# Optimization experiments

Measured on AMD Instinct MI355X. Metric: run time of the kernel, lower is better.

The kernel has to match this reference:

```python
import jax, jax.numpy as jnp
import numpy as np

EMBED = 1024
HEADS = 16
HEAD_DIM = EMBED // HEADS


def setup_inputs() -> dict:
    key = jax.random.key(0)
    ks = jax.random.split(key, 9)
    B, S, E = 4, 2048, EMBED
    std = 1.0 / np.sqrt(E)  # kaiming_normal fan_in, linear
    xav = np.sqrt(6.0 / (E + E))
    return {
        "x": jax.random.normal(ks[0], (B, S, E), dtype=jnp.float32),
        "Wq": jax.random.normal(ks[1], (E, E), dtype=jnp.float32) * std,
        "bq": jnp.zeros((E,), dtype=jnp.float32),
        "Wk": jax.random.normal(ks[2], (E, E), dtype=jnp.float32) * std,
        "bk": jnp.zeros((E,), dtype=jnp.float32),
        "Wv": jax.random.normal(ks[3], (E, E), dtype=jnp.float32) * std,
        "bv": jnp.zeros((E,), dtype=jnp.float32),
        "Wo": jax.random.uniform(ks[4], (E, E), dtype=jnp.float32, minval=-xav, maxval=xav),
        "bo": jnp.zeros((E,), dtype=jnp.float32),
        "ln_gamma": jnp.ones((E,), dtype=jnp.float32),
        "ln_beta": jnp.zeros((E,), dtype=jnp.float32),
    }


def _layer_norm(x, gamma, beta, eps=1e-5):
    mu = jnp.mean(x, axis=-1, keepdims=True)
    var = jnp.var(x, axis=-1, keepdims=True)
    return (x - mu) * jax.lax.rsqrt(var + eps) * gamma + beta


def reference(x, Wq, bq, Wk, bk, Wv, bv, Wo, bo, ln_gamma, ln_beta):
    B, S, E = x.shape
    residual = x
    h = _layer_norm(x, ln_gamma, ln_beta)
    # torch Linear: y = h @ W.T + b; here W stored as (out, in)
    Q = h @ Wq.T + bq
    K = h @ Wk.T + bk
    V = h @ Wv.T + bv
    # (B, H, S, D)
    def split(t):
        return t.reshape(B, S, HEADS, HEAD_DIM).transpose(0, 2, 1, 3)
    Q, K, V = split(Q), split(K), split(V)
    scale = HEAD_DIM ** -0.5
    scores = jnp.einsum("bhqd,bhkd->bhqk", Q, K) * scale  # (B,H,S,S)
    attn = jax.nn.softmax(scores.astype(jnp.float32), axis=-1).astype(scores.dtype)
    out = jnp.einsum("bhqk,bhkd->bhqd", attn, V)
    out = out.transpose(0, 2, 1, 3).reshape(B, S, E)
    out = out @ Wo.T + bo
    return out + residual
```

## Files before the change

kernel.cpp:

```cpp
#include <hip/hip_runtime.h>
#include <hip/hip_bf16.h>
#include <stdint.h>

#define EMB 1024
#define NH 16
#define HD 64
#define SEQ 2048
#define NB 4

typedef __attribute__((ext_vector_type(8))) short bh8;
typedef __attribute__((ext_vector_type(4))) float f32x4;

#define QSCALE 0.1803368801111f
#define SMAX_NEG -48.0f

__device__ __forceinline__ unsigned short f2bf(float x) {
  union { float f; uint32_t u; } v; v.f = x;
  uint32_t r = v.u + 0x7FFFu + ((v.u >> 16) & 1u);
  return (unsigned short)(r >> 16);
}

__device__ __forceinline__ void async16(void* lds, const void* g) {
  __builtin_amdgcn_global_load_lds(
      (const __attribute__((address_space(1))) uint32_t*)g,
      (__attribute__((address_space(3))) uint32_t*)lds,
      16, 0, 0);
}

#define MFMA_BF16(a, b, c) __builtin_amdgcn_mfma_f32_16x16x32_bf16((a), (b), (c), 0, 0, 0)

__global__ __launch_bounds__(256) void ln_kernel(const float* __restrict__ x,
                                                 const float* __restrict__ gamma,
                                                 const float* __restrict__ beta,
                                                 unsigned short* __restrict__ hout) {
  const int row = blockIdx.x;
  const int t = threadIdx.x;
  const float4 xv = ((const float4*)(x + (size_t)row * EMB))[t];
  float s = xv.x + xv.y + xv.z + xv.w;
  float ss = xv.x * xv.x + xv.y * xv.y + xv.z * xv.z + xv.w * xv.w;
#pragma unroll
  for (int off = 32; off; off >>= 1) {
    s += __shfl_down(s, off);
    ss += __shfl_down(ss, off);
  }
  __shared__ float red[8];
  const int wid = t >> 6, lane = t & 63;
  if (lane == 0) { red[wid] = s; red[4 + wid] = ss; }
  __syncthreads();
  const float S = red[0] + red[1] + red[2] + red[3];
  const float SS = red[4] + red[5] + red[6] + red[7];
  const float mu = S * (1.0f / EMB);
  const float var = SS * (1.0f / EMB) - mu * mu;
  const float rstd = rsqrtf(var + 1e-5f);
  const float4 gv = ((const float4*)gamma)[t];
  const float4 bv = ((const float4*)beta)[t];
  ushort4 o = make_ushort4(f2bf((xv.x - mu) * rstd * gv.x + bv.x),
                           f2bf((xv.y - mu) * rstd * gv.y + bv.y),
                           f2bf((xv.z - mu) * rstd * gv.z + bv.z),
                           f2bf((xv.w - mu) * rstd * gv.w + bv.w));
  ((ushort4*)(hout + (size_t)row * EMB))[t] = o;
}

__global__ __launch_bounds__(256) void prep_kernel(const float* __restrict__ Wq, const float* __restrict__ Wk,
                                                   const float* __restrict__ Wv, const float* __restrict__ Wo,
                                                   const float* __restrict__ bq, const float* __restrict__ bk,
                                                   const float* __restrict__ bv,
                                                   unsigned short* __restrict__ wcat,
                                                   unsigned short* __restrict__ wo,
                                                   float* __restrict__ bcat) {
  const int b = blockIdx.x;
  const int t = threadIdx.x;
  if (b < 3072) {
    const int i = b * 1024 + t * 4;
    const int proj = i >> 20;
    const int rem = i & 0xFFFFF;
    const float* src = (proj == 0) ? Wq : ((proj == 1) ? Wk : Wv);
    const float4 v = *(const float4*)(src + rem);
    *(ushort4*)(wcat + i) = make_ushort4(f2bf(v.x), f2bf(v.y), f2bf(v.z), f2bf(v.w));
  } else if (b < 4096) {
    const int i = (b - 3072) * 1024 + t * 4;
    const float4 v = *(const float4*)(Wo + i);
    *(ushort4*)(wo + i) = make_ushort4(f2bf(v.x), f2bf(v.y), f2bf(v.z), f2bf(v.w));
  } else {
    const int i = (b - 4096) * 1024 + t * 4;
    const int proj = i >> 10;
    const int rem = i & 1023;
    const float* src = (proj == 0) ? bq : ((proj == 1) ? bk : bv);
    const float4 v = *(const float4*)(src + rem);
    *(float4*)(bcat + i) = v;
  }
}

template <int EPI>
__global__ __launch_bounds__(256) void gemm_bt(const unsigned short* __restrict__ A,
                                               const unsigned short* __restrict__ B,
                                               int M, int N, int K, int mtiles,
                                               const float* __restrict__ bias,
                                               const float* __restrict__ resid,
                                               unsigned short* __restrict__ outq,
                                               float* __restrict__ outf) {
  __shared__ unsigned short Asm_[128 * 32];
  __shared__ unsigned short Bsm_[128 * 32];
  const int mt = blockIdx.x % mtiles;
  const int nt = blockIdx.x / mtiles;
  const int m0 = mt * 128, n0 = nt * 128;
  const int t = threadIdx.x;
  const int w = t >> 6, l = t & 63;
  const int wr = w >> 1, wc = w & 1;
  const int rlo = l & 15, rhi = l >> 4;

  f32x4 acc[4][4] = {};

  const int srow = (l >> 2);
  const int scol = (l & 3) * 8;

  for (int k0 = 0; k0 < K; k0 += 32) {
#pragma unroll
    for (int cc = 0; cc < 2; ++cc) {
      const int c = 2 * w + cc;
      const int row = c * 16 + srow;
      async16(&Asm_[c * 512 + l * 8], &A[(size_t)(m0 + row) * K + k0 + scol]);
      async16(&Bsm_[c * 512 + l * 8], &B[(size_t)(n0 + row) * K + k0 + scol]);
    }
    __syncthreads();
    bh8 af[4], bfr[4];
#pragma unroll
    for (int i = 0; i < 4; ++i)
      af[i] = *(const bh8*)&Asm_[(wr * 64 + i * 16 + rlo) * 32 + rhi * 8];
#pragma unroll
    for (int i = 0; i < 4; ++i)
      bfr[i] = *(const bh8*)&Bsm_[(wc * 64 + i * 16 + rlo) * 32 + rhi * 8];
#pragma unroll
    for (int i = 0; i < 4; ++i)
#pragma unroll
      for (int j = 0; j < 4; ++j)
        acc[i][j] = MFMA_BF16(af[i], bfr[j], acc[i][j]);
    __syncthreads();
  }

#pragma unroll
  for (int i = 0; i < 4; ++i)
#pragma unroll
    for (int j = 0; j < 4; ++j) {
      const int col = n0 + wc * 64 + j * 16 + rlo;
      const float bias_v = bias[col];
#pragma unroll
      for (int r = 0; r < 4; ++r) {
        const int row = m0 + wr * 64 + i * 16 + rhi * 4 + r;
        float v = acc[i][j][r] + bias_v;
        if (EPI == 0) {
          const int proj = col >> 10;
          if (proj == 0) v *= QSCALE;
          const int rem = col & 1023;
          const int hh = rem >> 6, d = rem & 63;
          const int bb = row >> 11, ss = row & 2047;
          outq[(size_t)proj * 8388608 + (((size_t)(bb * 16 + hh) * 2048 + ss) << 6) + d] = f2bf(v);
        } else {
          const size_t idx = (size_t)row * N + col;
          outf[idx] = v + resid[idx];
        }
      }
    }
}

__device__ __forceinline__ void stage_k(const unsigned short* __restrict__ Kb, size_t base,
                                        int kt, unsigned short* Ksm, int w, int l) {
#pragma unroll
  for (int cc = 0; cc < 2; ++cc) {
    const int c = 2 * w + cc;
    const int key = c * 8 + (l >> 3);
    const int colb = ((l & 7) * 16) ^ ((key & 7) << 4);
    async16(&((char*)Ksm)[c * 1024 + l * 16],
            (const char*)&Kb[base + (size_t)(kt * 64 + key) * HD] + colb);
  }
}

__device__ __forceinline__ void load_v(const unsigned short* __restrict__ Vb, size_t base,
                                       int kt, int m, int voct, bh8* v0, bh8* v1) {
  const int k0 = ((m & 1) << 5) + (m >> 1);
  const unsigned short* vsrc = &Vb[base + (size_t)(kt * 64 + k0) * HD + voct * 8];
  *v0 = *(const bh8*)vsrc;
  *v1 = *(const bh8*)(vsrc + 16 * HD);
}

__device__ __forceinline__ void write_v(unsigned short* Vsm, int m, int voct, bh8 v0, bh8 v1) {
  uint32_t* V32 = (uint32_t*)Vsm;
#pragma unroll
  for (int i = 0; i < 8; ++i) {
    const int d = voct * 8 + i;
    const uint32_t pk = (uint32_t)(unsigned short)v0[i] | ((uint32_t)(unsigned short)v1[i] << 16);
    V32[d * 32 + (m ^ ((d & 7) << 2))] = pk;
  }
}

__global__ __launch_bounds__(256) void attn_kernel(const unsigned short* __restrict__ Qb,
                                                   const unsigned short* __restrict__ Kb,
                                                   const unsigned short* __restrict__ Vb,
                                                   unsigned short* __restrict__ Ob) {
  __shared__ unsigned short Ksm[2][64 * 64];
  __shared__ unsigned short Vsm[2][64 * 64];
  __shared__ unsigned short Psm[4][16 * 64];

  const int lb = ((blockIdx.x & 7) << 8) | (blockIdx.x >> 3);
  const int qt = lb & 31;
  const int bh = lb >> 5;
  const int t = threadIdx.x, w = t >> 6, l = t & 63;
  const int rlo = l & 15, rhi = l >> 4;
  const int q0 = qt * 64 + w * 16;
  const size_t base = (size_t)bh * SEQ * HD;

  bh8 qa[2];
#pragma unroll
  for (int ds = 0; ds < 2; ++ds)
    qa[ds] = *(const bh8*)&Qb[base + (size_t)(q0 + rlo) * HD + ds * 32 + rhi * 8];

  f32x4 o[4] = {};
  float psum[4] = {0.0f, 0.0f, 0.0f, 0.0f};

  const int vm = t & 31;
  const int voct = t >> 5;

  stage_k(Kb, base, 0, Ksm[0], w, l);
  {
    bh8 v0, v1;
    load_v(Vb, base, 0, vm, voct, &v0, &v1);
    write_v(Vsm[0], vm, voct, v0, v1);
  }
  __syncthreads();

  for (int kt = 0; kt < 32; ++kt) {
    const int cur = kt & 1;
    bh8 nv0, nv1;
    if (kt < 31) {
      stage_k(Kb, base, kt + 1, Ksm[cur ^ 1], w, l);
      load_v(Vb, base, kt + 1, vm, voct, &nv0, &nv1);
    }

    const unsigned short* Kc = Ksm[cur];
    f32x4 sc[4];
#pragma unroll
    for (int kb = 0; kb < 4; ++kb) {
      const int key = kb * 16 + rlo;
      f32x4 a = {SMAX_NEG, SMAX_NEG, SMAX_NEG, SMAX_NEG};
#pragma unroll
      for (int ds = 0; ds < 2; ++ds) {
        const int colb = (ds * 64 + rhi * 16) ^ ((key & 7) << 4);
        const bh8 kf = *(const bh8*)&((const char*)Kc)[key * 128 + colb];
        a = MFMA_BF16(qa[ds], kf, a);
      }
      sc[kb] = a;
    }

#pragma unroll
    for (int kb = 0; kb < 4; ++kb)
#pragma unroll
      for (int r = 0; r < 4; ++r) {
        const float p = __builtin_amdgcn_exp2f(sc[kb][r]);
        sc[kb][r] = p;
        psum[r] += p;
      }

    {
      uint32_t* P32 = (uint32_t*)Psm[w];
#pragma unroll
      for (int r = 0; r < 4; ++r) {
        const int q = rhi * 4 + r;
        const int rowb = q * 32;
        const int sw = (q & 7) << 2;
        union { __hip_bfloat162 b; uint32_t u; } p0, p1;
        p0.b = __float22bfloat162_rn(make_float2(sc[0][r], sc[1][r]));
        p1.b = __float22bfloat162_rn(make_float2(sc[2][r], sc[3][r]));
        P32[rowb + ((2 * rlo) ^ sw)] = p0.u;
        P32[rowb + ((2 * rlo + 1) ^ sw)] = p1.u;
      }
    }

    const unsigned short* Pw = (const unsigned short*)Psm[w];
    bh8 pa[2];
#pragma unroll
    for (int ks = 0; ks < 2; ++ks) {
      const int colb = (ks * 64 + rhi * 16) ^ ((rlo & 7) << 4);
      pa[ks] = *(const bh8*)&((const char*)Pw)[rlo * 128 + colb];
    }

    const unsigned short* Vc = Vsm[cur];
#pragma unroll
    for (int ks = 0; ks < 2; ++ks)
#pragma unroll
      for (int df = 0; df < 4; ++df) {
        const int d = df * 16 + rlo;
        const int colb = (ks * 64 + rhi * 16) ^ ((d & 7) << 4);
        const bh8 vf = *(const bh8*)&((const char*)Vc)[d * 128 + colb];
        o[df] = MFMA_BF16(pa[ks], vf, o[df]);
      }

    if (kt < 31) write_v(Vsm[cur ^ 1], vm, voct, nv0, nv1);

    __syncthreads();
  }

#pragma unroll
  for (int r = 0; r < 4; ++r) {
#pragma unroll
    for (int off = 1; off < 16; off <<= 1) psum[r] += __shfl_xor(psum[r], off);
  }

#pragma unroll
  for (int r = 0; r < 4; ++r) {
    const float inv = 1.0f / psum[r];
    const int q = q0 + rhi * 4 + r;
    const size_t nrow = (size_t)(bh >> 4) * SEQ + q;
    const int hcol = (bh & 15) * HD;
#pragma unroll
    for (int df = 0; df < 4; ++df)
      Ob[nrow * EMB + hcol + df * 16 + rlo] = f2bf(o[df][r] * inv);
  }
}

extern "C" void kernel_launch(void* const* d_in, const int* in_sizes, int n_in,
                              void* d_out, int out_size, void* d_ws, size_t ws_size,
                              hipStream_t stream) {
  const float* x = (const float*)d_in[0];
  const float* Wq = (const float*)d_in[1];
  const float* bq = (const float*)d_in[2];
  const float* Wk = (const float*)d_in[3];
  const float* bk = (const float*)d_in[4];
  const float* Wv = (const float*)d_in[5];
  const float* bv = (const float*)d_in[6];
  const float* Wo = (const float*)d_in[7];
  const float* bo = (const float*)d_in[8];
  const float* gamma = (const float*)d_in[9];
  const float* beta = (const float*)d_in[10];

  char* ws = (char*)d_ws;
  unsigned short* h = (unsigned short*)(ws);
  unsigned short* wcat = (unsigned short*)(ws + (16u << 20));
  unsigned short* wo = (unsigned short*)(ws + (22u << 20));
  float* bcat = (float*)(ws + (24u << 20));
  unsigned short* qkv = (unsigned short*)(ws + (25u << 20));
  unsigned short* aout = h;
  float* out = (float*)d_out;

  ln_kernel<<<dim3(8192), dim3(256), 0, stream>>>(x, gamma, beta, h);
  prep_kernel<<<dim3(4099), dim3(256), 0, stream>>>(Wq, Wk, Wv, Wo, bq, bk, bv, wcat, wo, bcat);
  gemm_bt<0><<<dim3(64 * 24), dim3(256), 0, stream>>>(h, wcat, 8192, 3072, 1024, 64,
                                                      bcat, nullptr, qkv, nullptr);
  attn_kernel<<<dim3(2048), dim3(256), 0, stream>>>(qkv, qkv + 8388608, qkv + 16777216, aout);
  gemm_bt<1><<<dim3(64 * 8), dim3(256), 0, stream>>>(aout, wo, 8192, 1024, 1024, 64,
                                                     bo, x, nullptr, out);
}
```

Baseline: 333.0 us.

## Double attention query tile per block and vectorize GEMM epilogue stores

The attention kernel now handles 128 queries per block (32 per wave, two 16-row groups) instead of 64, so each K/V tile staged in LDS serves twice as many MFMAs. The grid is halved to match. Separately, the GEMM swaps MFMA operand order so each lane holds four consecutive output columns, which lets the epilogue do float4 bias/residual loads and ushort4/float4 stores. The trade-off is more registers per wave in attention and fewer blocks in flight.

Result: no change. 338.8 us (+1.7%).

```diff
diff --git a/kernel.cpp b/kernel.cpp
--- a/kernel.cpp
+++ b/kernel.cpp
@@ -134,33 +134,36 @@
     for (int i = 0; i < 4; ++i)
 #pragma unroll
       for (int j = 0; j < 4; ++j)
-        acc[i][j] = MFMA_BF16(af[i], bfr[j], acc[i][j]);
+        acc[i][j] = MFMA_BF16(bfr[j], af[i], acc[i][j]);
     __syncthreads();
   }
 
 #pragma unroll
-  for (int i = 0; i < 4; ++i)
-#pragma unroll
-    for (int j = 0; j < 4; ++j) {
-      const int col = n0 + wc * 64 + j * 16 + rlo;
-      const float bias_v = bias[col];
-#pragma unroll
-      for (int r = 0; r < 4; ++r) {
-        const int row = m0 + wr * 64 + i * 16 + rhi * 4 + r;
-        float v = acc[i][j][r] + bias_v;
-        if (EPI == 0) {
-          const int proj = col >> 10;
-          if (proj == 0) v *= QSCALE;
-          const int rem = col & 1023;
-          const int hh = rem >> 6, d = rem & 63;
-          const int bb = row >> 11, ss = row & 2047;
-          outq[(size_t)proj * 8388608 + (((size_t)(bb * 16 + hh) * 2048 + ss) << 6) + d] = f2bf(v);
-        } else {
-          const size_t idx = (size_t)row * N + col;
-          outf[idx] = v + resid[idx];
-        }
-      }
-    }
+  for (int j = 0; j < 4; ++j) {
+    const int ncb = n0 + wc * 64 + j * 16 + rhi * 4;
+    const float4 bv4 = *(const float4*)&bias[ncb];
+#pragma unroll
+    for (int i = 0; i < 4; ++i) {
+      const int row = m0 + wr * 64 + i * 16 + rlo;
+      float v0 = acc[i][j][0] + bv4.x;
+      float v1 = acc[i][j][1] + bv4.y;
+      float v2 = acc[i][j][2] + bv4.z;
+      float v3 = acc[i][j][3] + bv4.w;
+      if (EPI == 0) {
+        const int proj = ncb >> 10;
+        if (proj == 0) { v0 *= QSCALE; v1 *= QSCALE; v2 *= QSCALE; v3 *= QSCALE; }
+        const int rem = ncb & 1023;
+        const int hh = rem >> 6, d = rem & 63;
+        const int bb = row >> 11, ss = row & 2047;
+        const ushort4 pk = make_ushort4(f2bf(v0), f2bf(v1), f2bf(v2), f2bf(v3));
+        *(ushort4*)&outq[(size_t)proj * 8388608 + (((size_t)(bb * 16 + hh) * 2048 + ss) << 6) + d] = pk;
+      } else {
+        const size_t idx = (size_t)row * N + ncb;
+        const float4 rv = *(const float4*)&resid[idx];
+        *(float4*)&outf[idx] = make_float4(v0 + rv.x, v1 + rv.y, v2 + rv.z, v3 + rv.w);
+      }
+    }
+  }
 }
 
 __device__ __forceinline__ void stage_k(const unsigned short* __restrict__ Kb, size_t base,
@@ -201,21 +204,23 @@
   __shared__ unsigned short Vsm[2][64 * 64];
   __shared__ unsigned short Psm[4][16 * 64];
 
-  const int lb = ((blockIdx.x & 7) << 8) | (blockIdx.x >> 3);
-  const int qt = lb & 31;
-  const int bh = lb >> 5;
+  const int lb = ((blockIdx.x & 7) << 7) | (blockIdx.x >> 3);
+  const int qt = lb & 15;
+  const int bh = lb >> 4;
   const int t = threadIdx.x, w = t >> 6, l = t & 63;
   const int rlo = l & 15, rhi = l >> 4;
-  const int q0 = qt * 64 + w * 16;
+  const int q0 = qt * 128 + w * 32;
   const size_t base = (size_t)bh * SEQ * HD;
 
-  bh8 qa[2];
-#pragma unroll
-  for (int ds = 0; ds < 2; ++ds)
-    qa[ds] = *(const bh8*)&Qb[base + (size_t)(q0 + rlo) * HD + ds * 32 + rhi * 8];
-
-  f32x4 o[4] = {};
-  float psum[4] = {0.0f, 0.0f, 0.0f, 0.0f};
+  bh8 qa[2][2];
+#pragma unroll
+  for (int g = 0; g < 2; ++g)
+#pragma unroll
+    for (int ds = 0; ds < 2; ++ds)
+      qa[g][ds] = *(const bh8*)&Qb[base + (size_t)(q0 + g * 16 + rlo) * HD + ds * 32 + rhi * 8];
+
+  f32x4 o[2][4] = {};
+  float psum[2][4] = {};
 
   const int vm = t & 31;
   const int voct = t >> 5;
@@ -237,50 +242,51 @@
     }
 
     const unsigned short* Kc = Ksm[cur];
-    f32x4 sc[4];
+    f32x4 sc[2][4];
+#pragma unroll
+    for (int kb = 0; kb < 4; ++kb) {
+      sc[0][kb] = f32x4{SMAX_NEG, SMAX_NEG, SMAX_NEG, SMAX_NEG};
+      sc[1][kb] = f32x4{SMAX_NEG, SMAX_NEG, SMAX_NEG, SMAX_NEG};
+    }
 #pragma unroll
     for (int kb = 0; kb < 4; ++kb) {
       const int key = kb * 16 + rlo;
-      f32x4 a = {SMAX_NEG, SMAX_NEG, SMAX_NEG, SMAX_NEG};
 #pragma unroll
       for (int ds = 0; ds < 2; ++ds) {
         const int colb = (ds * 64 + rhi * 16) ^ ((key & 7) << 4);
         const bh8 kf = *(const bh8*)&((const char*)Kc)[key * 128 + colb];
-        a = MFMA_BF16(qa[ds], kf, a);
-      }
-      sc[kb] = a;
-    }
-
-#pragma unroll
-    for (int kb = 0; kb < 4; ++kb)
-#pragma unroll
-      for (int r = 0; r < 4; ++r) {
-        const float p = __builtin_amdgcn_exp2f(sc[kb][r]);
-        sc[kb][r] = p;
-        psum[r] += p;
-      }
-
-    {
-      uint32_t* P32 = (uint32_t*)Psm[w];
+        sc[0][kb] = MFMA_BF16(qa[0][ds], kf, sc[0][kb]);
+        sc[1][kb] = MFMA_BF16(qa[1][ds], kf, sc[1][kb]);
+      }
+    }
+
+    uint32_t* P32 = (uint32_t*)Psm[w];
+    const unsigned short* Pw = (const unsigned short*)Psm[w];
+    bh8 pa[2][2];
+#pragma unroll
+    for (int g = 0; g < 2; ++g) {
+#pragma unroll
+      for (int kb = 0; kb < 4; ++kb)
+#pragma unroll
+        for (int r = 0; r < 4; ++r) {
+          const float p = __builtin_amdgcn_exp2f(sc[g][kb][r]);
+          sc[g][kb][r] = p;
+          psum[g][r] += p;
+        }
 #pragma unroll
       for (int r = 0; r < 4; ++r) {
         const int q = rhi * 4 + r;
-        const int rowb = q * 32;
-        const int sw = (q & 7) << 2;
+        const int e = (2 * rlo) ^ ((q & 7) << 2);
         union { __hip_bfloat162 b; uint32_t u; } p0, p1;
-        p0.b = __float22bfloat162_rn(make_float2(sc[0][r], sc[1][r]));
-        p1.b = __float22bfloat162_rn(make_float2(sc[2][r], sc[3][r]));
-        P32[rowb + ((2 * rlo) ^ sw)] = p0.u;
-        P32[rowb + ((2 * rlo + 1) ^ sw)] = p1.u;
-      }
-    }
-
-    const unsigned short* Pw = (const unsigned short*)Psm[w];
-    bh8 pa[2];
-#pragma unroll
-    for (int ks = 0; ks < 2; ++ks) {
-      const int colb = (ks * 64 + rhi * 16) ^ ((rlo & 7) << 4);
-      pa[ks] = *(const bh8*)&((const char*)Pw)[rlo * 128 + colb];
+        p0.b = __float22bfloat162_rn(make_float2(sc[g][0][r], sc[g][1][r]));
+        p1.b = __float22bfloat162_rn(make_float2(sc[g][2][r], sc[g][3][r]));
+        *(uint2*)((char*)P32 + q * 128 + e * 4) = make_uint2(p0.u, p1.u);
+      }
+#pragma unroll
+      for (int ks = 0; ks < 2; ++ks) {
+        const int colb = (ks * 64 + rhi * 16) ^ ((rlo & 7) << 4);
+        pa[g][ks] = *(const bh8*)&((const char*)Pw)[rlo * 128 + colb];
+      }
     }
 
     const unsigned short* Vc = Vsm[cur];
@@ -291,7 +297,8 @@
         const int d = df * 16 + rlo;
         const int colb = (ks * 64 + rhi * 16) ^ ((d & 7) << 4);
         const bh8 vf = *(const bh8*)&((const char*)Vc)[d * 128 + colb];
-        o[df] = MFMA_BF16(pa[ks], vf, o[df]);
+        o[0][df] = MFMA_BF16(pa[0][ks], vf, o[0][df]);
+        o[1][df] = MFMA_BF16(pa[1][ks], vf, o[1][df]);
       }
 
     if (kt < 31) write_v(Vsm[cur ^ 1], vm, voct, nv0, nv1);
@@ -300,21 +307,25 @@
   }
 
 #pragma unroll
-  for (int r = 0; r < 4; ++r) {
-#pragma unroll
-    for (int off = 1; off < 16; off <<= 1) psum[r] += __shfl_xor(psum[r], off);
-  }
-
-#pragma unroll
-  for (int r = 0; r < 4; ++r) {
-    const float inv = 1.0f / psum[r];
-    const int q = q0 + rhi * 4 + r;
-    const size_t nrow = (size_t)(bh >> 4) * SEQ + q;
-    const int hcol = (bh & 15) * HD;
-#pragma unroll
-    for (int df = 0; df < 4; ++df)
-      Ob[nrow * EMB + hcol + df * 16 + rlo] = f2bf(o[df][r] * inv);
-  }
+  for (int g = 0; g < 2; ++g)
+#pragma unroll
+    for (int r = 0; r < 4; ++r) {
+#pragma unroll
+      for (int off = 1; off < 16; off <<= 1) psum[g][r] += __shfl_xor(psum[g][r], off);
+    }
+
+  const size_t brow = (size_t)(bh >> 4) * SEQ;
+  const int hcol = (bh & 15) * HD;
+#pragma unroll
+  for (int g = 0; g < 2; ++g)
+#pragma unroll
+    for (int r = 0; r < 4; ++r) {
+      const float inv = 1.0f / psum[g][r];
+      const int q = q0 + g * 16 + rhi * 4 + r;
+#pragma unroll
+      for (int df = 0; df < 4; ++df)
+        Ob[(brow + q) * EMB + hcol + df * 16 + rlo] = f2bf(o[g][df][r] * inv);
+    }
 }
 
 extern "C" void kernel_launch(void* const* d_in, const int* in_sizes, int n_in,
@@ -345,7 +356,7 @@
   prep_kernel<<<dim3(4099), dim3(256), 0, stream>>>(Wq, Wk, Wv, Wo, bq, bk, bv, wcat, wo, bcat);
   gemm_bt<0><<<dim3(64 * 24), dim3(256), 0, stream>>>(h, wcat, 8192, 3072, 1024, 64,
                                                       bcat, nullptr, qkv, nullptr);
-  attn_kernel<<<dim3(2048), dim3(256), 0, stream>>>(qkv, qkv + 8388608, qkv + 16777216, aout);
+  attn_kernel<<<dim3(1024), dim3(256), 0, stream>>>(qkv, qkv + 8388608, qkv + 16777216, aout);
   gemm_bt<1><<<dim3(64 * 8), dim3(256), 0, stream>>>(aout, wo, 8192, 1024, 1024, 64,
                                                      bo, x, nullptr, out);
 }
```
